# Kernel optimization log

Measured on AMD Instinct MI355X. Metric: run time of the kernel, lower is better.

Reference implementation:

```python
import jax, jax.numpy as jnp
import numpy as np

D_MODEL, N_HEAD, N_KV_HEAD, D_HEAD = 1024, 16, 4, 64


def rotate_half(x):
    x1, x2 = x[..., : x.shape[-1] // 2], x[..., x.shape[-1] // 2:]
    return jnp.concatenate((-x2, x1), axis=-1)


def rope_cos_sin(seq_len, dim, dtype=jnp.float32):
    inv_freq = 1.0 / (10000.0 ** (jnp.arange(0, dim, 2, dtype=jnp.float32) / dim))
    t = jnp.arange(seq_len, dtype=jnp.float32)
    freqs = jnp.einsum('i,j->ij', t, inv_freq)          # [S, dim/2]
    emb = jnp.concatenate((freqs, freqs), axis=-1)       # [S, dim]
    return jnp.cos(emb).astype(dtype), jnp.sin(emb).astype(dtype)


def setup_inputs() -> dict:
    key = jax.random.key(0)
    ks = jax.random.split(key, 5)
    B, S = 2, 2048
    scale = 0.02
    return {
        'x': jax.random.normal(ks[0], (B, S, D_MODEL), dtype=jnp.float32),
        'Wq': jax.random.normal(ks[1], (D_MODEL, N_HEAD * D_HEAD), dtype=jnp.float32) * scale,
        'Wk': jax.random.normal(ks[2], (D_MODEL, N_KV_HEAD * D_HEAD), dtype=jnp.float32) * scale,
        'Wv': jax.random.normal(ks[3], (D_MODEL, N_KV_HEAD * D_HEAD), dtype=jnp.float32) * scale,
        'Wo': jax.random.normal(ks[4], (N_HEAD * D_HEAD, D_MODEL), dtype=jnp.float32) * scale,
    }


def reference(x, Wq, Wk, Wv, Wo):
    B, S, _ = x.shape
    scale = 1.0 / np.sqrt(D_HEAD)
    # projections -> [B, H, S, Dh]
    q = (x @ Wq).reshape(B, S, N_HEAD, D_HEAD).transpose(0, 2, 1, 3)
    k = (x @ Wk).reshape(B, S, N_KV_HEAD, D_HEAD).transpose(0, 2, 1, 3)
    v = (x @ Wv).reshape(B, S, N_KV_HEAD, D_HEAD).transpose(0, 2, 1, 3)
    cos, sin = rope_cos_sin(S, D_HEAD, x.dtype)          # [S, Dh]
    q = q * cos + rotate_half(q) * sin
    k = k * cos + rotate_half(k) * sin
    rep = N_HEAD // N_KV_HEAD
    k = jnp.repeat(k, rep, axis=1)                       # [B, H, S, Dh]
    v = jnp.repeat(v, rep, axis=1)
    scores = jnp.einsum('bhqd,bhkd->bhqk', q, k) * scale # [B, H, S, S]
    causal = jnp.triu(jnp.ones((S, S), dtype=bool), k=1)
    scores = jnp.where(causal, -jnp.inf, scores)
    probs = jax.nn.softmax(scores, axis=-1)
    ctx = jnp.einsum('bhqk,bhkd->bhqd', probs, v)        # [B, H, S, Dh]
    ctx = ctx.transpose(0, 2, 1, 3).reshape(B, S, N_HEAD * D_HEAD)
    return ctx @ Wo
```

## Files before the change

kernel.cpp:

```cpp
#include <hip/hip_runtime.h>
#include <hip/hip_bf16.h>
#include <cstdint>
#include <math.h>

#define S_LEN 2048
#define DM 1024
#define NQKV 1536
#define MROWS 4096
#define BKT 64

typedef __attribute__((ext_vector_type(8))) short short8;
typedef __attribute__((ext_vector_type(4))) float f32x4;
typedef __attribute__((ext_vector_type(16))) float f32x16;

#define QFOLD 0.18033688011112042f

__device__ __forceinline__ short f2bf(float x) {
  union { float f; uint32_t u; } v; v.f = x;
  uint32_t r = (v.u + 0x7fffu + ((v.u >> 16) & 1u)) >> 16;
  return (short)(uint16_t)r;
}

__device__ __forceinline__ uint32_t pk2(float a, float b) {
  __hip_bfloat162 h = __float22bfloat162_rn(make_float2(a, b));
  union { __hip_bfloat162 h2; uint32_t u; } cv; cv.h2 = h;
  return cv.u;
}

__global__ __launch_bounds__(256) void prep(const float* __restrict__ x,
    const float* __restrict__ Wq, const float* __restrict__ Wk,
    const float* __restrict__ Wv, const float* __restrict__ Wo,
    short* __restrict__ Xb, short* __restrict__ WcatT, short* __restrict__ WoT) {
  __shared__ short T[64 * 72];
  const int bb = blockIdx.x;
  const int tid = threadIdx.x;
  if (bb < 4096) {
    const int i = bb * 256 + tid;
    float4 v = ((const float4*)x)[i];
    short4 o;
    o.x = f2bf(v.x); o.y = f2bf(v.y); o.z = f2bf(v.z); o.w = f2bf(v.w);
    ((short4*)Xb)[i] = o;
    return;
  }
  const float* src; short* dst; int R, C, t2 = bb - 4096;
  if (t2 < 256)      { src = Wq; dst = WcatT;                        R = 1024; C = 1024; }
  else if (t2 < 320) { t2 -= 256; src = Wk; dst = WcatT + (size_t)1024*1024; R = 1024; C = 256; }
  else if (t2 < 384) { t2 -= 320; src = Wv; dst = WcatT + (size_t)1280*1024; R = 1024; C = 256; }
  else               { t2 -= 384; src = Wo; dst = WoT;               R = 1024; C = 1024; }
  const int r0 = (t2 & 15) * 64, c0 = (t2 >> 4) * 64;
  #pragma unroll
  for (int i = 0; i < 4; ++i) {
    int chunk = tid + i * 256;
    int r = chunk >> 4, cc = (chunk & 15) * 4;
    float4 v = *(const float4*)&src[(size_t)(r0 + r) * C + c0 + cc];
    T[(cc + 0) * 72 + r] = f2bf(v.x);
    T[(cc + 1) * 72 + r] = f2bf(v.y);
    T[(cc + 2) * 72 + r] = f2bf(v.z);
    T[(cc + 3) * 72 + r] = f2bf(v.w);
  }
  __syncthreads();
  #pragma unroll
  for (int i = 0; i < 2; ++i) {
    int chunk = tid + i * 256;
    int rr = chunk >> 3, kk = (chunk & 7) * 8;
    *(uint4*)&dst[(size_t)(c0 + rr) * R + r0 + kk] = *(uint4*)&T[rr * 72 + kk];
  }
}

template<int BMT, int BNT>
__global__ __launch_bounds__(256) void gemm_bf16_t(const short* __restrict__ A,
    const short* __restrict__ BT, float* __restrict__ C, int M, int N, int K) {
  constexpr int MI = BMT / 32, NI = BNT / 32;
  __shared__ short As[BMT * BKT];
  __shared__ short Bs[BNT * BKT];
  const int tid = threadIdx.x;
  const int wave = tid >> 6, lane = tid & 63;
  const int quad = lane >> 4, l15 = lane & 15;
  const int wm = (wave >> 1) * (BMT / 2), wn = (wave & 1) * (BNT / 2);
  const int m0 = blockIdx.y * BMT, n0 = blockIdx.x * BNT;
  const int rA = wave * (BMT / 4) + (lane >> 3);
  const int rB = wave * (BNT / 4) + (lane >> 3);
  const int scol = (lane & 7) * 8;

  f32x4 acc[MI][NI] = {};

  for (int k0 = 0; k0 < K; k0 += BKT) {
    __syncthreads();
    #pragma unroll
    for (int j = 0; j < MI; ++j)
      __builtin_amdgcn_global_load_lds(
          (const __attribute__((address_space(1))) void*)&A[(size_t)(m0 + rA + j * 8) * K + k0 + scol],
          (__attribute__((address_space(3))) void*)&As[(wave * MI + j) * 512],
          16, 0, 0);
    #pragma unroll
    for (int j = 0; j < NI; ++j)
      __builtin_amdgcn_global_load_lds(
          (const __attribute__((address_space(1))) void*)&BT[(size_t)(n0 + rB + j * 8) * K + k0 + scol],
          (__attribute__((address_space(3))) void*)&Bs[(wave * NI + j) * 512],
          16, 0, 0);
    __syncthreads();
    #pragma unroll
    for (int ks = 0; ks < 2; ++ks) {
      short8 af[MI], bfr[NI];
      #pragma unroll
      for (int mi = 0; mi < MI; ++mi)
        af[mi] = *(const short8*)&As[(wm + mi*16 + l15)*BKT + ks*32 + quad*8];
      #pragma unroll
      for (int ni = 0; ni < NI; ++ni)
        bfr[ni] = *(const short8*)&Bs[(wn + ni*16 + l15)*BKT + ks*32 + quad*8];
      #pragma unroll
      for (int mi = 0; mi < MI; ++mi)
        #pragma unroll
        for (int ni = 0; ni < NI; ++ni)
          acc[mi][ni] = __builtin_amdgcn_mfma_f32_16x16x32_bf16(af[mi], bfr[ni], acc[mi][ni], 0, 0, 0);
    }
  }
  #pragma unroll
  for (int mi = 0; mi < MI; ++mi)
    #pragma unroll
    for (int ni = 0; ni < NI; ++ni)
      #pragma unroll
      for (int r = 0; r < 4; ++r)
        C[(size_t)(m0 + wm + mi*16 + quad*4 + r)*N + (n0 + wn + ni*16 + l15)] = acc[mi][ni][r];
}

__global__ void rope_kernel(const float* __restrict__ qkv, short* __restrict__ Qb,
                            short* __restrict__ Kb, short* __restrict__ Vb) {
  __shared__ float csn[64];
  const int row = blockIdx.x;
  const int s = row & (S_LEN - 1);
  const int tid = threadIdx.x;
  const float* rp = qkv + (size_t)row * NQKV;
  if (tid < 32) {
    float inv = exp2f(-(float)tid * 0.41524101186092029f);
    float ang = (float)s * inv;
    csn[tid] = cosf(ang);
    csn[tid + 32] = sinf(ang);
  }
  __syncthreads();
  #pragma unroll
  for (int i = 0; i < 2; ++i) {
    int p = tid + i * 256;
    int hh = p >> 5, j = p & 31;
    float cs = csn[j], sn = csn[j + 32];
    float x1 = rp[hh*64 + j], x2 = rp[hh*64 + j + 32];
    Qb[(size_t)row*1024 + hh*64 + j]      = f2bf((x1*cs - x2*sn) * QFOLD);
    Qb[(size_t)row*1024 + hh*64 + j + 32] = f2bf((x2*cs + x1*sn) * QFOLD);
  }
  if (tid < 128) {
    int hh = tid >> 5, j = tid & 31;
    float cs = csn[j], sn = csn[j + 32];
    float x1 = rp[1024 + hh*64 + j], x2 = rp[1024 + hh*64 + j + 32];
    const int sw = (s & 7) << 3;
    Kb[(size_t)row*256 + hh*64 + (j ^ sw)]        = f2bf(x1*cs - x2*sn);
    Kb[(size_t)row*256 + hh*64 + ((j + 32) ^ sw)] = f2bf(x2*cs + x1*sn);
  }
  Vb[(size_t)row*256 + tid] = f2bf(rp[1280 + tid]);
}

__global__ __launch_bounds__(256) void transpose_v(const short* __restrict__ Vb,
                                                   short* __restrict__ Vt) {
  __shared__ short T[64 * 72];
  const int s0 = blockIdx.x * 64;
  const int bh = blockIdx.y;
  const int b = bh >> 2, kvh = bh & 3;
  const int tid = threadIdx.x;
  #pragma unroll
  for (int i = 0; i < 2; ++i) {
    int chunk = tid + i * 256;
    int r = chunk >> 3, c = (chunk & 7) * 8;
    short8 v = *(const short8*)&Vb[(size_t)(b*S_LEN + s0 + r)*256 + kvh*64 + c];
    #pragma unroll
    for (int t = 0; t < 8; ++t) T[(c + t) * 72 + r] = v[t];
  }
  __syncthreads();
  #pragma unroll
  for (int i = 0; i < 2; ++i) {
    int chunk = tid + i * 256;
    int rr = chunk >> 3, kk = (chunk & 7) * 8;
    *(uint4*)&Vt[(size_t)(bh*64 + rr)*S_LEN + s0 + (kk ^ ((rr & 7) << 3))] = *(uint4*)&T[rr * 72 + kk];
  }
}

__global__ __launch_bounds__(256, 2) void fattn10(const short* __restrict__ Qb,
    const short* __restrict__ Kb, const short* __restrict__ Vt, short* __restrict__ Ctx) {
  __shared__ short SMEM[32768];
  const int idx = blockIdx.x;
  const int pi  = idx & 15;
  const int h   = (idx >> 4) & 15;
  const int b   = idx >> 8;
  const int kvh = h >> 2;
  const int tid = threadIdx.x, wav = tid >> 6, lane = tid & 63;
  const int l31 = lane & 31, hi = lane >> 5;
  const int qs = wav & 1, g = wav >> 1;
  const int sx = (l31 & 7) << 3;
  const size_t qbase  = (size_t)b * S_LEN * 1024;
  const size_t kbase  = (size_t)b * S_LEN * 256;
  const size_t vtbase = (size_t)(b * 4 + kvh) * 64 * S_LEN;

  const short* kptr = Kb + kbase + (size_t)(wav * 16 + (lane >> 3)) * 256 + kvh * 64 + (lane & 7) * 8;
  const short* vptr = Vt + vtbase + (size_t)(wav * 16 + (lane >> 3)) * 2048 + (lane & 7) * 8;

#define STAGE(u) do { \
    const int bi_ = (u) & 3; \
    const short* kp_ = kptr + (size_t)(u) * 16384; \
    const short* vp_ = vptr + (u) * 64; \
    short* kd_ = &SMEM[bi_ * 8192 + wav * 1024]; \
    short* vd_ = &SMEM[bi_ * 8192 + 4096 + wav * 1024]; \
    _Pragma("unroll") \
    for (int i_ = 0; i_ < 2; ++i_) { \
      __builtin_amdgcn_global_load_lds((const __attribute__((address_space(1))) void*)(kp_ + i_ * 2048), \
          (__attribute__((address_space(3))) void*)(kd_ + i_ * 512), 16, 0, 0); \
      __builtin_amdgcn_global_load_lds((const __attribute__((address_space(1))) void*)(vp_ + i_ * 16384), \
          (__attribute__((address_space(3))) void*)(vd_ + i_ * 512), 16, 0, 0); \
    } \
  } while (0)

  for (int half = 0; half < 2; ++half) {
    const int jt = half ? (31 - pi) : pi;
    const int q0 = jt * 64;
    const int ntiles = jt + 1;
    const int qg = q0 + qs * 32 + l31;

    short8 qf[4];
    {
      const short* qp = &Qb[qbase + (size_t)qg * 1024 + h * 64 + hi * 8];
      #pragma unroll
      for (int ks = 0; ks < 4; ++ks) qf[ks] = *(const short8*)(qp + ks * 16);
    }

    f32x16 O0 = {}, O1 = {};
    float la0 = 0.f, la1 = 0.f, la2 = 0.f, la3 = 0.f;

    STAGE(0);
    if (ntiles > 1) STAGE(1);
    if (ntiles > 2) STAGE(2);

    for (int t = 0; t < ntiles; ++t) {
      const int k0 = t * 64;
      const int rem = ntiles - 1 - t;
      if (rem >= 2)      { asm volatile("s_waitcnt vmcnt(8)" ::: "memory"); }
      else if (rem == 1) { asm volatile("s_waitcnt vmcnt(4)" ::: "memory"); }
      else               { asm volatile("s_waitcnt vmcnt(0)" ::: "memory"); }
      __builtin_amdgcn_sched_barrier(0);
      __builtin_amdgcn_s_barrier();
      if (t + 3 < ntiles) STAGE(t + 3);

      const short* ks_ = &SMEM[(t & 3) * 8192];
      const short* vs_ = &SMEM[(t & 3) * 8192 + 4096];

      f32x16 sc;
      __builtin_amdgcn_s_setprio(1);
      {
        const int r = g * 32 + l31;
        f32x16 a = {};
        #pragma unroll
        for (int ks2 = 0; ks2 < 4; ++ks2) {
          short8 kf = *(const short8*)&ks_[r * 64 + ((ks2 * 16 + hi * 8) ^ sx)];
          a = __builtin_amdgcn_mfma_f32_32x32x16_bf16(kf, qf[ks2], a, 0, 0, 0);
        }
        sc = a;
      }
      __builtin_amdgcn_s_setprio(0);

      if (t == ntiles - 1) {
        #pragma unroll
        for (int r = 0; r < 16; ++r) {
          const int kvg = k0 + g * 32 + (r & 3) + 8 * (r >> 2) + 4 * hi;
          if (kvg > qg) sc[r] = -1e30f;
        }
      }

      short8 af[2];
      {
        #pragma unroll
        for (int r = 0; r < 16; ++r) sc[r] = exp2f(sc[r]);
        la0 += (sc[0] + sc[1]) + (sc[2] + sc[3]);
        la1 += (sc[4] + sc[5]) + (sc[6] + sc[7]);
        la2 += (sc[8] + sc[9]) + (sc[10] + sc[11]);
        la3 += (sc[12] + sc[13]) + (sc[14] + sc[15]);
        #pragma unroll
        for (int st = 0; st < 2; ++st) {
          uint32_t x0 = pk2(sc[st * 8 + 0], sc[st * 8 + 1]);
          uint32_t x1 = pk2(sc[st * 8 + 2], sc[st * 8 + 3]);
          uint32_t x2 = pk2(sc[st * 8 + 4], sc[st * 8 + 5]);
          uint32_t x3 = pk2(sc[st * 8 + 6], sc[st * 8 + 7]);
          asm("v_permlane32_swap_b32 %0, %1" : "+v"(x0), "+v"(x2));
          asm("v_permlane32_swap_b32 %0, %1" : "+v"(x1), "+v"(x3));
          union { short8 s8; uint32_t u[4]; } cv;
          cv.u[0] = x0; cv.u[1] = x1; cv.u[2] = x2; cv.u[3] = x3;
          af[st] = cv.s8;
        }
      }

      __builtin_amdgcn_s_setprio(1);
      #pragma unroll
      for (int s2 = 0; s2 < 2; ++s2) {
        const int co = g * 32 + s2 * 16 + hi * 8;
        short8 bv0 = *(const short8*)&vs_[l31 * 64 + (co ^ sx)];
        O0 = __builtin_amdgcn_mfma_f32_32x32x16_bf16(af[s2], bv0, O0, 0, 0, 0);
        short8 bv1 = *(const short8*)&vs_[(32 + l31) * 64 + (co ^ sx)];
        O1 = __builtin_amdgcn_mfma_f32_32x32x16_bf16(af[s2], bv1, O1, 0, 0, 0);
      }
      __builtin_amdgcn_s_setprio(0);
    }

    float ll = (la0 + la1) + (la2 + la3);
    ll += __shfl_xor(ll, 32, 64);
    __syncthreads();

    float* Os = (float*)SMEM;
    float* Ls = (float*)SMEM + 2 * 64 * 33;
    if (g == 1) {
      float* op = &Os[(qs * 64 + lane) * 33];
      #pragma unroll
      for (int r = 0; r < 16; ++r) { op[r] = O0[r]; op[16 + r] = O1[r]; }
      Ls[qs * 64 + lane] = ll;
    }
    __syncthreads();
    if (g == 0) {
      const float* op = &Os[(qs * 64 + lane) * 33];
      ll += Ls[qs * 64 + lane];
      #pragma unroll
      for (int r = 0; r < 16; ++r) { O0[r] += op[r]; O1[r] += op[16 + r]; }
      const float inv = 1.0f / ll;
      #pragma unroll
      for (int r = 0; r < 16; ++r) {
        const int crow = (r & 3) + 8 * (r >> 2) + 4 * hi;
        const float invr = __shfl(inv, crow, 64);
        const size_t o = qbase + (size_t)(q0 + qs * 32 + crow) * 1024 + h * 64;
        Ctx[o + l31]      = f2bf(O0[r] * invr);
        Ctx[o + 32 + l31] = f2bf(O1[r] * invr);
      }
    }
    __syncthreads();
  }
#undef STAGE
}

extern "C" void kernel_launch(void* const* d_in, const int* in_sizes, int n_in,
                              void* d_out, int out_size, void* d_ws, size_t ws_size,
                              hipStream_t stream) {
  const float* x  = (const float*)d_in[0];
  const float* Wq = (const float*)d_in[1];
  const float* Wk = (const float*)d_in[2];
  const float* Wv = (const float*)d_in[3];
  const float* Wo = (const float*)d_in[4];
  float* out = (float*)d_out;

  char* w = (char*)d_ws;
  short* Xb    = (short*)w;  w += (size_t)MROWS * DM * 2;
  short* WcatT = (short*)w;  w += (size_t)NQKV * DM * 2;
  short* WoT   = (short*)w;  w += (size_t)DM * DM * 2;
  float* QKVf  = (float*)w;  w += (size_t)MROWS * NQKV * 4;
  short* Qbuf  = (short*)w;  w += (size_t)MROWS * DM * 2;
  short* Kbuf  = (short*)w;  w += (size_t)MROWS * 256 * 2;
  short* Vbuf  = (short*)w;  w += (size_t)MROWS * 256 * 2;
  short* Vt    = (short*)w;  w += (size_t)8 * 64 * S_LEN * 2;
  short* Ctx   = (short*)QKVf;

  prep<<<dim3(4736), dim3(256), 0, stream>>>(x, Wq, Wk, Wv, Wo, Xb, WcatT, WoT);

  gemm_bf16_t<64,128><<<dim3(NQKV / 128, MROWS / 64), dim3(256), 0, stream>>>(Xb, WcatT, QKVf, MROWS, NQKV, DM);
  rope_kernel<<<dim3(MROWS), dim3(256), 0, stream>>>(QKVf, Qbuf, Kbuf, Vbuf);
  transpose_v<<<dim3(32, 8), dim3(256), 0, stream>>>(Vbuf, Vt);
  fattn10<<<dim3(512), dim3(256), 0, stream>>>(Qbuf, Kbuf, Vt, Ctx);
  gemm_bf16_t<64,128><<<dim3(DM / 128, MROWS / 64), dim3(256), 0, stream>>>(Ctx, WoT, out, MROWS, DM, DM);
}
```

Before: 178.4 us.

## Fuse RoPE into QKV GEMM epilogue and rebalance attention grid

The QKV GEMM now applies RoPE, the softmax scale fold, the K swizzle and the bf16 conversion in its epilogue, using a cos/sin table precomputed in prep. This removes the fp32 QKV intermediate and the separate rope kernel launch. The attention kernel changes from 512 blocks that each process a paired light and heavy query tile to 1024 blocks with one query tile each, ordered heaviest first. It uses triple instead of quadruple LDS buffering to allow 3 blocks per CU. This trades the built-in causal load balancing for more occupancy and relies on the heavy-first ordering to balance the tail.

```diff
diff --git a/kernel.cpp b/kernel.cpp
--- a/kernel.cpp
+++ b/kernel.cpp
@@ -30,7 +30,8 @@
 __global__ __launch_bounds__(256) void prep(const float* __restrict__ x,
     const float* __restrict__ Wq, const float* __restrict__ Wk,
     const float* __restrict__ Wv, const float* __restrict__ Wo,
-    short* __restrict__ Xb, short* __restrict__ WcatT, short* __restrict__ WoT) {
+    short* __restrict__ Xb, short* __restrict__ WcatT, short* __restrict__ WoT,
+    float2* __restrict__ tab) {
   __shared__ short T[64 * 72];
   const int bb = blockIdx.x;
   const int tid = threadIdx.x;
@@ -40,6 +41,18 @@
     short4 o;
     o.x = f2bf(v.x); o.y = f2bf(v.y); o.z = f2bf(v.z); o.w = f2bf(v.w);
     ((short4*)Xb)[i] = o;
+    return;
+  }
+  if (bb >= 4736) {
+    const int gid = (bb - 4736) * 256 + tid;
+    #pragma unroll
+    for (int e = 0; e < 4; ++e) {
+      const int ii = gid + e * 16384;
+      const int s = ii >> 5, j = ii & 31;
+      const float inv = exp2f(-(float)j * 0.41524101186092029f);
+      const float ang = (float)s * inv;
+      tab[ii] = make_float2(cosf(ang), sinf(ang));
+    }
     return;
   }
   const float* src; short* dst; int R, C, t2 = bb - 4096;
@@ -124,38 +137,101 @@
         C[(size_t)(m0 + wm + mi*16 + quad*4 + r)*N + (n0 + wn + ni*16 + l15)] = acc[mi][ni][r];
 }
 
-__global__ void rope_kernel(const float* __restrict__ qkv, short* __restrict__ Qb,
-                            short* __restrict__ Kb, short* __restrict__ Vb) {
-  __shared__ float csn[64];
-  const int row = blockIdx.x;
-  const int s = row & (S_LEN - 1);
+__global__ __launch_bounds__(256, 3) void gemm_qkv(const short* __restrict__ A,
+    const short* __restrict__ BT, const float2* __restrict__ tab,
+    short* __restrict__ Qb, short* __restrict__ Kb, short* __restrict__ Vb) {
+  constexpr int MI = 2, NI = 4;
+  __shared__ short As[64 * BKT];
+  __shared__ short Bs[128 * BKT];
   const int tid = threadIdx.x;
-  const float* rp = qkv + (size_t)row * NQKV;
-  if (tid < 32) {
-    float inv = exp2f(-(float)tid * 0.41524101186092029f);
-    float ang = (float)s * inv;
-    csn[tid] = cosf(ang);
-    csn[tid + 32] = sinf(ang);
-  }
-  __syncthreads();
-  #pragma unroll
-  for (int i = 0; i < 2; ++i) {
-    int p = tid + i * 256;
-    int hh = p >> 5, j = p & 31;
-    float cs = csn[j], sn = csn[j + 32];
-    float x1 = rp[hh*64 + j], x2 = rp[hh*64 + j + 32];
-    Qb[(size_t)row*1024 + hh*64 + j]      = f2bf((x1*cs - x2*sn) * QFOLD);
-    Qb[(size_t)row*1024 + hh*64 + j + 32] = f2bf((x2*cs + x1*sn) * QFOLD);
-  }
-  if (tid < 128) {
-    int hh = tid >> 5, j = tid & 31;
-    float cs = csn[j], sn = csn[j + 32];
-    float x1 = rp[1024 + hh*64 + j], x2 = rp[1024 + hh*64 + j + 32];
-    const int sw = (s & 7) << 3;
-    Kb[(size_t)row*256 + hh*64 + (j ^ sw)]        = f2bf(x1*cs - x2*sn);
-    Kb[(size_t)row*256 + hh*64 + ((j + 32) ^ sw)] = f2bf(x2*cs + x1*sn);
-  }
-  Vb[(size_t)row*256 + tid] = f2bf(rp[1280 + tid]);
+  const int wave = tid >> 6, lane = tid & 63;
+  const int quad = lane >> 4, l15 = lane & 15;
+  const int wm = (wave >> 1) * 32, wn = (wave & 1) * 64;
+  const int m0 = blockIdx.y * 64, n0 = blockIdx.x * 128;
+  const int rA = wave * 16 + (lane >> 3);
+  const int rB = wave * 32 + (lane >> 3);
+  const int scol = (lane & 7) * 8;
+
+  f32x4 acc[MI][NI] = {};
+
+  for (int k0 = 0; k0 < DM; k0 += BKT) {
+    __syncthreads();
+    #pragma unroll
+    for (int j = 0; j < MI; ++j)
+      __builtin_amdgcn_global_load_lds(
+          (const __attribute__((address_space(1))) void*)&A[(size_t)(m0 + rA + j * 8) * DM + k0 + scol],
+          (__attribute__((address_space(3))) void*)&As[(wave * MI + j) * 512],
+          16, 0, 0);
+    #pragma unroll
+    for (int j = 0; j < NI; ++j)
+      __builtin_amdgcn_global_load_lds(
+          (const __attribute__((address_space(1))) void*)&BT[(size_t)(n0 + rB + j * 8) * DM + k0 + scol],
+          (__attribute__((address_space(3))) void*)&Bs[(wave * NI + j) * 512],
+          16, 0, 0);
+    __syncthreads();
+    #pragma unroll
+    for (int ks = 0; ks < 2; ++ks) {
+      short8 af[MI], bfr[NI];
+      #pragma unroll
+      for (int mi = 0; mi < MI; ++mi)
+        af[mi] = *(const short8*)&As[(wm + mi*16 + l15)*BKT + ks*32 + quad*8];
+      #pragma unroll
+      for (int ni = 0; ni < NI; ++ni)
+        bfr[ni] = *(const short8*)&Bs[(wn + ni*16 + l15)*BKT + ks*32 + quad*8];
+      #pragma unroll
+      for (int mi = 0; mi < MI; ++mi)
+        #pragma unroll
+        for (int ni = 0; ni < NI; ++ni)
+          acc[mi][ni] = __builtin_amdgcn_mfma_f32_16x16x32_bf16(af[mi], bfr[ni], acc[mi][ni], 0, 0, 0);
+    }
+  }
+
+  const int c0 = n0 + wn;
+  if (n0 < 1024) {
+    #pragma unroll
+    for (int mi = 0; mi < MI; ++mi)
+      #pragma unroll
+      for (int r = 0; r < 4; ++r) {
+        const int row = m0 + wm + mi*16 + quad*4 + r;
+        const int s = row & (S_LEN - 1);
+        #pragma unroll
+        for (int ni = 0; ni < 2; ++ni) {
+          const int j = ni*16 + l15;
+          const float2 cn = tab[s*32 + j];
+          const float x1 = acc[mi][ni][r], x2 = acc[mi][ni+2][r];
+          Qb[(size_t)row*1024 + c0 + j]      = f2bf((x1*cn.x - x2*cn.y) * QFOLD);
+          Qb[(size_t)row*1024 + c0 + j + 32] = f2bf((x2*cn.x + x1*cn.y) * QFOLD);
+        }
+      }
+  } else if (n0 < 1280) {
+    const int hh = (c0 - 1024) >> 6;
+    #pragma unroll
+    for (int mi = 0; mi < MI; ++mi)
+      #pragma unroll
+      for (int r = 0; r < 4; ++r) {
+        const int row = m0 + wm + mi*16 + quad*4 + r;
+        const int s = row & (S_LEN - 1);
+        const int sw = (s & 7) << 3;
+        #pragma unroll
+        for (int ni = 0; ni < 2; ++ni) {
+          const int j = ni*16 + l15;
+          const float2 cn = tab[s*32 + j];
+          const float x1 = acc[mi][ni][r], x2 = acc[mi][ni+2][r];
+          Kb[(size_t)row*256 + hh*64 + (j ^ sw)]        = f2bf(x1*cn.x - x2*cn.y);
+          Kb[(size_t)row*256 + hh*64 + ((j + 32) ^ sw)] = f2bf(x2*cn.x + x1*cn.y);
+        }
+      }
+  } else {
+    #pragma unroll
+    for (int mi = 0; mi < MI; ++mi)
+      #pragma unroll
+      for (int ni = 0; ni < NI; ++ni)
+        #pragma unroll
+        for (int r = 0; r < 4; ++r) {
+          const int row = m0 + wm + mi*16 + quad*4 + r;
+          Vb[(size_t)row*256 + (c0 - 1280) + ni*16 + l15] = f2bf(acc[mi][ni][r]);
+        }
+  }
 }
 
 __global__ __launch_bounds__(256) void transpose_v(const short* __restrict__ Vb,
@@ -182,13 +258,13 @@
   }
 }
 
-__global__ __launch_bounds__(256, 2) void fattn10(const short* __restrict__ Qb,
+__global__ __launch_bounds__(256, 3) void fattn11(const short* __restrict__ Qb,
     const short* __restrict__ Kb, const short* __restrict__ Vt, short* __restrict__ Ctx) {
-  __shared__ short SMEM[32768];
+  __shared__ short SMEM[24576];
   const int idx = blockIdx.x;
-  const int pi  = idx & 15;
-  const int h   = (idx >> 4) & 15;
-  const int b   = idx >> 8;
+  const int h   = idx & 15;
+  const int b   = (idx >> 4) & 1;
+  const int jt  = 31 - (idx >> 5);
   const int kvh = h >> 2;
   const int tid = threadIdx.x, wav = tid >> 6, lane = tid & 63;
   const int l31 = lane & 31, hi = lane >> 5;
@@ -202,7 +278,7 @@
   const short* vptr = Vt + vtbase + (size_t)(wav * 16 + (lane >> 3)) * 2048 + (lane & 7) * 8;
 
 #define STAGE(u) do { \
-    const int bi_ = (u) & 3; \
+    const int bi_ = (u) % 3; \
     const short* kp_ = kptr + (size_t)(u) * 16384; \
     const short* vp_ = vptr + (u) * 64; \
     short* kd_ = &SMEM[bi_ * 8192 + wav * 1024]; \
@@ -216,124 +292,118 @@
     } \
   } while (0)
 
-  for (int half = 0; half < 2; ++half) {
-    const int jt = half ? (31 - pi) : pi;
-    const int q0 = jt * 64;
-    const int ntiles = jt + 1;
-    const int qg = q0 + qs * 32 + l31;
-
-    short8 qf[4];
+  const int q0 = jt * 64;
+  const int ntiles = jt + 1;
+  const int qg = q0 + qs * 32 + l31;
+
+  short8 qf[4];
+  {
+    const short* qp = &Qb[qbase + (size_t)qg * 1024 + h * 64 + hi * 8];
+    #pragma unroll
+    for (int ks = 0; ks < 4; ++ks) qf[ks] = *(const short8*)(qp + ks * 16);
+  }
+
+  f32x16 O0 = {}, O1 = {};
+  float la0 = 0.f, la1 = 0.f, la2 = 0.f, la3 = 0.f;
+
+  STAGE(0);
+  if (ntiles > 1) STAGE(1);
+
+  for (int t = 0; t < ntiles; ++t) {
+    const int k0 = t * 64;
+    const int rem = ntiles - 1 - t;
+    if (rem >= 1) { asm volatile("s_waitcnt vmcnt(4)" ::: "memory"); }
+    else          { asm volatile("s_waitcnt vmcnt(0)" ::: "memory"); }
+    __builtin_amdgcn_sched_barrier(0);
+    __builtin_amdgcn_s_barrier();
+    if (t + 2 < ntiles) STAGE(t + 2);
+
+    const short* ks_ = &SMEM[(t % 3) * 8192];
+    const short* vs_ = &SMEM[(t % 3) * 8192 + 4096];
+
+    f32x16 sc;
+    __builtin_amdgcn_s_setprio(1);
     {
-      const short* qp = &Qb[qbase + (size_t)qg * 1024 + h * 64 + hi * 8];
-      #pragma unroll
-      for (int ks = 0; ks < 4; ++ks) qf[ks] = *(const short8*)(qp + ks * 16);
-    }
-
-    f32x16 O0 = {}, O1 = {};
-    float la0 = 0.f, la1 = 0.f, la2 = 0.f, la3 = 0.f;
-
-    STAGE(0);
-    if (ntiles > 1) STAGE(1);
-    if (ntiles > 2) STAGE(2);
-
-    for (int t = 0; t < ntiles; ++t) {
-      const int k0 = t * 64;
-      const int rem = ntiles - 1 - t;
-      if (rem >= 2)      { asm volatile("s_waitcnt vmcnt(8)" ::: "memory"); }
-      else if (rem == 1) { asm volatile("s_waitcnt vmcnt(4)" ::: "memory"); }
-      else               { asm volatile("s_waitcnt vmcnt(0)" ::: "memory"); }
-      __builtin_amdgcn_sched_barrier(0);
-      __builtin_amdgcn_s_barrier();
-      if (t + 3 < ntiles) STAGE(t + 3);
-
-      const short* ks_ = &SMEM[(t & 3) * 8192];
-      const short* vs_ = &SMEM[(t & 3) * 8192 + 4096];
-
-      f32x16 sc;
-      __builtin_amdgcn_s_setprio(1);
-      {
-        const int r = g * 32 + l31;
-        f32x16 a = {};
-        #pragma unroll
-        for (int ks2 = 0; ks2 < 4; ++ks2) {
-          short8 kf = *(const short8*)&ks_[r * 64 + ((ks2 * 16 + hi * 8) ^ sx)];
-          a = __builtin_amdgcn_mfma_f32_32x32x16_bf16(kf, qf[ks2], a, 0, 0, 0);
-        }
-        sc = a;
+      const int r = g * 32 + l31;
+      f32x16 a = {};
+      #pragma unroll
+      for (int ks2 = 0; ks2 < 4; ++ks2) {
+        short8 kf = *(const short8*)&ks_[r * 64 + ((ks2 * 16 + hi * 8) ^ sx)];
+        a = __builtin_amdgcn_mfma_f32_32x32x16_bf16(kf, qf[ks2], a, 0, 0, 0);
       }
-      __builtin_amdgcn_s_setprio(0);
-
-      if (t == ntiles - 1) {
-        #pragma unroll
-        for (int r = 0; r < 16; ++r) {
-          const int kvg = k0 + g * 32 + (r & 3) + 8 * (r >> 2) + 4 * hi;
-          if (kvg > qg) sc[r] = -1e30f;
-        }
+      sc = a;
+    }
+    __builtin_amdgcn_s_setprio(0);
+
+    if (t == ntiles - 1) {
+      #pragma unroll
+      for (int r = 0; r < 16; ++r) {
+        const int kvg = k0 + g * 32 + (r & 3) + 8 * (r >> 2) + 4 * hi;
+        if (kvg > qg) sc[r] = -1e30f;
       }
-
-      short8 af[2];
-      {
-        #pragma unroll
-        for (int r = 0; r < 16; ++r) sc[r] = exp2f(sc[r]);
-        la0 += (sc[0] + sc[1]) + (sc[2] + sc[3]);
-        la1 += (sc[4] + sc[5]) + (sc[6] + sc[7]);
-        la2 += (sc[8] + sc[9]) + (sc[10] + sc[11]);
-        la3 += (sc[12] + sc[13]) + (sc[14] + sc[15]);
-        #pragma unroll
-        for (int st = 0; st < 2; ++st) {
-          uint32_t x0 = pk2(sc[st * 8 + 0], sc[st * 8 + 1]);
-          uint32_t x1 = pk2(sc[st * 8 + 2], sc[st * 8 + 3]);
-          uint32_t x2 = pk2(sc[st * 8 + 4], sc[st * 8 + 5]);
-          uint32_t x3 = pk2(sc[st * 8 + 6], sc[st * 8 + 7]);
-          asm("v_permlane32_swap_b32 %0, %1" : "+v"(x0), "+v"(x2));
-          asm("v_permlane32_swap_b32 %0, %1" : "+v"(x1), "+v"(x3));
-          union { short8 s8; uint32_t u[4]; } cv;
-          cv.u[0] = x0; cv.u[1] = x1; cv.u[2] = x2; cv.u[3] = x3;
-          af[st] = cv.s8;
-        }
+    }
+
+    short8 af[2];
+    {
+      #pragma unroll
+      for (int r = 0; r < 16; ++r) sc[r] = exp2f(sc[r]);
+      la0 += (sc[0] + sc[1]) + (sc[2] + sc[3]);
+      la1 += (sc[4] + sc[5]) + (sc[6] + sc[7]);
+      la2 += (sc[8] + sc[9]) + (sc[10] + sc[11]);
+      la3 += (sc[12] + sc[13]) + (sc[14] + sc[15]);
+      #pragma unroll
+      for (int st = 0; st < 2; ++st) {
+        uint32_t x0 = pk2(sc[st * 8 + 0], sc[st * 8 + 1]);
+        uint32_t x1 = pk2(sc[st * 8 + 2], sc[st * 8 + 3]);
+        uint32_t x2 = pk2(sc[st * 8 + 4], sc[st * 8 + 5]);
+        uint32_t x3 = pk2(sc[st * 8 + 6], sc[st * 8 + 7]);
+        asm("v_permlane32_swap_b32 %0, %1" : "+v"(x0), "+v"(x2));
+        asm("v_permlane32_swap_b32 %0, %1" : "+v"(x1), "+v"(x3));
+        union { short8 s8; uint32_t u[4]; } cv;
+        cv.u[0] = x0; cv.u[1] = x1; cv.u[2] = x2; cv.u[3] = x3;
+        af[st] = cv.s8;
       }
-
-      __builtin_amdgcn_s_setprio(1);
-      #pragma unroll
-      for (int s2 = 0; s2 < 2; ++s2) {
-        const int co = g * 32 + s2 * 16 + hi * 8;
-        short8 bv0 = *(const short8*)&vs_[l31 * 64 + (co ^ sx)];
-        O0 = __builtin_amdgcn_mfma_f32_32x32x16_bf16(af[s2], bv0, O0, 0, 0, 0);
-        short8 bv1 = *(const short8*)&vs_[(32 + l31) * 64 + (co ^ sx)];
-        O1 = __builtin_amdgcn_mfma_f32_32x32x16_bf16(af[s2], bv1, O1, 0, 0, 0);
-      }
-      __builtin_amdgcn_s_setprio(0);
-    }
-
-    float ll = (la0 + la1) + (la2 + la3);
-    ll += __shfl_xor(ll, 32, 64);
-    __syncthreads();
-
-    float* Os = (float*)SMEM;
-    float* Ls = (float*)SMEM + 2 * 64 * 33;
-    if (g == 1) {
-      float* op = &Os[(qs * 64 + lane) * 33];
-      #pragma unroll
-      for (int r = 0; r < 16; ++r) { op[r] = O0[r]; op[16 + r] = O1[r]; }
-      Ls[qs * 64 + lane] = ll;
-    }
-    __syncthreads();
-    if (g == 0) {
-      const float* op = &Os[(qs * 64 + lane) * 33];
-      ll += Ls[qs * 64 + lane];
-      #pragma unroll
-      for (int r = 0; r < 16; ++r) { O0[r] += op[r]; O1[r] += op[16 + r]; }
-      const float inv = 1.0f / ll;
-      #pragma unroll
-      for (int r = 0; r < 16; ++r) {
-        const int crow = (r & 3) + 8 * (r >> 2) + 4 * hi;
-        const float invr = __shfl(inv, crow, 64);
-        const size_t o = qbase + (size_t)(q0 + qs * 32 + crow) * 1024 + h * 64;
-        Ctx[o + l31]      = f2bf(O0[r] * invr);
-        Ctx[o + 32 + l31] = f2bf(O1[r] * invr);
-      }
-    }
-    __syncthreads();
+    }
+
+    __builtin_amdgcn_s_setprio(1);
+    #pragma unroll
+    for (int s2 = 0; s2 < 2; ++s2) {
+      const int co = g * 32 + s2 * 16 + hi * 8;
+      short8 bv0 = *(const short8*)&vs_[l31 * 64 + (co ^ sx)];
+      O0 = __builtin_amdgcn_mfma_f32_32x32x16_bf16(af[s2], bv0, O0, 0, 0, 0);
+      short8 bv1 = *(const short8*)&vs_[(32 + l31) * 64 + (co ^ sx)];
+      O1 = __builtin_amdgcn_mfma_f32_32x32x16_bf16(af[s2], bv1, O1, 0, 0, 0);
+    }
+    __builtin_amdgcn_s_setprio(0);
+  }
+
+  float ll = (la0 + la1) + (la2 + la3);
+  ll += __shfl_xor(ll, 32, 64);
+  __syncthreads();
+
+  float* Os = (float*)SMEM;
+  float* Ls = (float*)SMEM + 2 * 64 * 33;
+  if (g == 1) {
+    float* op = &Os[(qs * 64 + lane) * 33];
+    #pragma unroll
+    for (int r = 0; r < 16; ++r) { op[r] = O0[r]; op[16 + r] = O1[r]; }
+    Ls[qs * 64 + lane] = ll;
+  }
+  __syncthreads();
+  if (g == 0) {
+    const float* op = &Os[(qs * 64 + lane) * 33];
+    ll += Ls[qs * 64 + lane];
+    #pragma unroll
+    for (int r = 0; r < 16; ++r) { O0[r] += op[r]; O1[r] += op[16 + r]; }
+    const float inv = 1.0f / ll;
+    #pragma unroll
+    for (int r = 0; r < 16; ++r) {
+      const int crow = (r & 3) + 8 * (r >> 2) + 4 * hi;
+      const float invr = __shfl(inv, crow, 64);
+      const size_t o = qbase + (size_t)(q0 + qs * 32 + crow) * 1024 + h * 64;
+      Ctx[o + l31]      = f2bf(O0[r] * invr);
+      Ctx[o + 32 + l31] = f2bf(O1[r] * invr);
+    }
   }
 #undef STAGE
 }
@@ -349,21 +419,20 @@
   float* out = (float*)d_out;
 
   char* w = (char*)d_ws;
-  short* Xb    = (short*)w;  w += (size_t)MROWS * DM * 2;
-  short* WcatT = (short*)w;  w += (size_t)NQKV * DM * 2;
-  short* WoT   = (short*)w;  w += (size_t)DM * DM * 2;
-  float* QKVf  = (float*)w;  w += (size_t)MROWS * NQKV * 4;
-  short* Qbuf  = (short*)w;  w += (size_t)MROWS * DM * 2;
-  short* Kbuf  = (short*)w;  w += (size_t)MROWS * 256 * 2;
-  short* Vbuf  = (short*)w;  w += (size_t)MROWS * 256 * 2;
-  short* Vt    = (short*)w;  w += (size_t)8 * 64 * S_LEN * 2;
-  short* Ctx   = (short*)QKVf;
-
-  prep<<<dim3(4736), dim3(256), 0, stream>>>(x, Wq, Wk, Wv, Wo, Xb, WcatT, WoT);
-
-  gemm_bf16_t<64,128><<<dim3(NQKV / 128, MROWS / 64), dim3(256), 0, stream>>>(Xb, WcatT, QKVf, MROWS, NQKV, DM);
-  rope_kernel<<<dim3(MROWS), dim3(256), 0, stream>>>(QKVf, Qbuf, Kbuf, Vbuf);
+  short*  Xb    = (short*)w;   w += (size_t)MROWS * DM * 2;
+  short*  WcatT = (short*)w;   w += (size_t)NQKV * DM * 2;
+  short*  WoT   = (short*)w;   w += (size_t)DM * DM * 2;
+  short*  Qbuf  = (short*)w;   w += (size_t)MROWS * DM * 2;
+  short*  Kbuf  = (short*)w;   w += (size_t)MROWS * 256 * 2;
+  short*  Vbuf  = (short*)w;   w += (size_t)MROWS * 256 * 2;
+  short*  Vt    = (short*)w;   w += (size_t)8 * 64 * S_LEN * 2;
+  short*  Ctx   = (short*)w;   w += (size_t)MROWS * DM * 2;
+  float2* tab   = (float2*)w;  w += (size_t)S_LEN * 32 * 8;
+
+  prep<<<dim3(4800), dim3(256), 0, stream>>>(x, Wq, Wk, Wv, Wo, Xb, WcatT, WoT, tab);
+
+  gemm_qkv<<<dim3(NQKV / 128, MROWS / 64), dim3(256), 0, stream>>>(Xb, WcatT, tab, Qbuf, Kbuf, Vbuf);
   transpose_v<<<dim3(32, 8), dim3(256), 0, stream>>>(Vbuf, Vt);
-  fattn10<<<dim3(512), dim3(256), 0, stream>>>(Qbuf, Kbuf, Vt, Ctx);
+  fattn11<<<dim3(1024), dim3(256), 0, stream>>>(Qbuf, Kbuf, Vt, Ctx);
   gemm_bf16_t<64,128><<<dim3(DM / 128, MROWS / 64), dim3(256), 0, stream>>>(Ctx, WoT, out, MROWS, DM, DM);
 }
```

Result: faster. 164.5 us (-7.8%).
